# Kernel tuning notes

Hardware: AMD Instinct MI355X
Metric: run time of the kernel (lower is better)

The kernel has to match this reference:

```python
import jax, jax.numpy as jnp
import numpy as np

B, N, C, H, NL, NH = 8, 1024, 256, 512, 3, 8


def setup_inputs() -> dict:
    key = jax.random.key(0)
    ks = jax.random.split(key, 16)
    g = lambda k, shape: jax.random.normal(k, shape, jnp.float32) * 0.02
    return dict(
        concept_features=jax.random.normal(ks[0], (B, N, C), jnp.float32),
        adjacency_matrix=jax.random.uniform(ks[1], (B, N, N), jnp.float32),
        edge_types=jax.random.randint(ks[2], (B, N, N), 0, 10),
        concept_mask=jnp.ones((B, N), bool),
        W_emb=g(ks[3], (H, C)), b_emb=jnp.zeros((H,), jnp.float32),
        W_in=g(ks[4], (NL, 3 * H, H)), b_in=jnp.zeros((NL, 3 * H), jnp.float32),
        W_out=g(ks[5], (NL, H, H)), b_out=jnp.zeros((NL, H), jnp.float32),
        W_conv=g(ks[6], (NL, H, H)), b_conv=jnp.zeros((NL, H), jnp.float32),
        W_cls=g(ks[7], (1, H)), b_cls=jnp.zeros((1,), jnp.float32),
        W_diff=g(ks[8], (5, H)), b_diff=jnp.zeros((5,), jnp.float32),
        W_pre=g(ks[9], (1, 2 * H)), b_pre=jnp.zeros((1,), jnp.float32),
        W_pool=g(ks[10], (H, H)), b_pool=jnp.zeros((H,), jnp.float32),
    )


def reference(concept_features, adjacency_matrix, edge_types, concept_mask,
              W_emb, b_emb, W_in, b_in, W_out, b_out, W_conv, b_conv,
              W_cls, b_cls, W_diff, b_diff, W_pre, b_pre, W_pool, b_pool):
    Bq, Nc, _ = concept_features.shape
    Hd = W_emb.shape[0]
    dh = Hd // NH

    def mha(x, Wi, bi, Wo, bo):
        # torch nn.MultiheadAttention with batch_first=False: the (B,N,H)
        # input is treated as (seq=B, batch=N, embed=H) -> attention over B.
        qkv = x @ Wi.T + bi                      # (B,N,3H)
        q, k, v = jnp.split(qkv, 3, axis=-1)
        rs = lambda t: t.reshape(Bq, Nc, NH, dh)
        q, k, v = rs(q), rs(k), rs(v)
        sc = jnp.einsum('inhd,jnhd->nhij', q, k) / jnp.sqrt(jnp.float32(dh))
        a = jax.nn.softmax(sc, axis=-1)          # (N,NH,B,B)
        o = jnp.einsum('nhij,jnhd->inhd', a, v).reshape(Bq, Nc, Hd)
        return o @ Wo.T + bo

    def ln(x):  # F.layer_norm, no affine
        m = x.mean(-1, keepdims=True)
        v = ((x - m) ** 2).mean(-1, keepdims=True)
        return (x - m) * jax.lax.rsqrt(v + 1e-5)

    x = concept_features @ W_emb.T + b_emb       # (B,N,H)
    for l in range(W_in.shape[0]):
        att = mha(x, W_in[l], b_in[l], W_out[l], b_out[l])
        conv = att @ W_conv[l].T + b_conv[l]
        agg = jnp.einsum('bij,bjh->bih', adjacency_matrix, conv)
        x = ln(x + agg)

    mastery = x @ W_cls.T + b_cls                # (B,N,1)
    diff = x @ W_diff.T + b_diff                 # (B,N,5)

    # O(N^2) pairwise loop -> bilinear decomposition:
    # score(i,j) = x_i @ W_pre[:, :H].T + x_j @ W_pre[:, H:].T + b
    h1 = (x @ W_pre[:, :Hd].T)[..., 0]           # (B,N)
    h2 = (x @ W_pre[:, Hd:].T)[..., 0]           # (B,N)
    pair = h1[:, :, None] + h2[:, None, :] + b_pre[0]  # (B,N,N)
    off = ~np.eye(Nc, dtype=bool).reshape(-1)    # static mask, i!=j row-major
    prereq = pair.reshape(Bq, Nc * Nc)[:, off][..., None]  # (B,N*(N-1),1)

    graph = x.mean(axis=1) @ W_pool.T + b_pool   # (B,H)
    return (x, mastery, diff, prereq, graph)
```

## Files before the change

### kernel.cpp

```cpp
#include <hip/hip_runtime.h>
#include <hip/hip_bf16.h>

typedef unsigned short ushort_t;
typedef __attribute__((ext_vector_type(4))) float floatx4;
typedef __attribute__((ext_vector_type(8))) __bf16 bf16x8;
typedef __attribute__((ext_vector_type(4))) unsigned short ushortx4;
typedef __attribute__((ext_vector_type(8))) unsigned short ushortx8;

static __device__ __forceinline__ float b2f(ushort_t u) {
  union { unsigned int i; float f; } v; v.i = ((unsigned int)u) << 16; return v.f;
}
static __device__ __forceinline__ ushort_t f2b(float f) {
  unsigned int x = __float_as_uint(f);
  unsigned int r = (x + 0x7fffu + ((x >> 16) & 1u)) >> 16;
  return (ushort_t)r;
}
static __device__ __forceinline__ void glds16(const ushort_t* g, ushort_t* l) {
  __builtin_amdgcn_global_load_lds(
      (const __attribute__((address_space(1))) unsigned int*)g,
      (__attribute__((address_space(3))) unsigned int*)l, 16, 0, 0);
}

template<int MODE, bool ASPLIT, int KS>
__global__ __launch_bounds__(256, 3) void gemm_bt(
    const void* __restrict__ Ap, const ushort_t* __restrict__ Bm,
    const float* __restrict__ bias,
    ushort_t* __restrict__ C0, ushort_t* __restrict__ C1,
    ushort_t* __restrict__ C2, ushort_t* __restrict__ C3,
    int M, int N, int K, long aBatch, long bBatch, long cBatch)
{
  __shared__ __align__(16) ushort_t As[128 * 64];
  __shared__ __align__(16) ushort_t Bs[128 * 64];

  const int tid  = threadIdx.x;
  const int wid  = tid >> 6;
  const int lane = tid & 63;
  const int quad = lane >> 4;
  const int l16  = lane & 15;
  const int lin = blockIdx.y * gridDim.x + blockIdx.x;
  const int m0 = (lin % gridDim.y) * 128;
  const int n0 = (lin / gridDim.y) * 128;
  const int z  = (KS > 1) ? (int)(blockIdx.z / KS) : blockIdx.z;
  const int kq = (KS > 1) ? (int)(blockIdx.z % KS) : 0;
  const int kbeg = kq * (K / KS);
  const int kend = kbeg + (K / KS);
  ushort_t* outB = C0;
  if (KS >= 2 && kq == 1) outB = C1;
  if (KS >= 4 && kq == 2) outB = C2;
  if (KS >= 4 && kq == 3) outB = C3;

  const ushort_t* Ab = (const ushort_t*)Ap + (long)z * aBatch;
  const float*    Af = (const float*)Ap + (long)z * aBatch;
  Bm += (long)z * bBatch;

  const int wr = (wid >> 1) * 64;
  const int wc = (wid & 1) * 64;

  const int srow = tid >> 3;
  const int scj  = ((tid & 7) ^ (srow & 7)) * 8;
  const long abase = (long)(m0 + srow) * K + scj;
  const long bbase = (long)(n0 + srow) * K + scj;

  floatx4 acc[4][4];
#pragma unroll
  for (int i = 0; i < 4; ++i)
#pragma unroll
    for (int j = 0; j < 4; ++j) acc[i][j] = (floatx4){0.f, 0.f, 0.f, 0.f};

  const int rx = l16 & 7;

  for (int k0 = kbeg; k0 < kend; k0 += 64) {
    __syncthreads();
    if constexpr (ASPLIT) {
#pragma unroll
      for (int p = 0; p < 4; ++p)
        glds16(Ab + abase + 32 * p * (long)K + k0, &As[tid * 8 + p * 2048]);
    } else {
#pragma unroll
      for (int p = 0; p < 8; ++p) {
        int c = tid + p * 256;
        int row = c >> 4, sub4 = c & 15;
        floatx4 va = *(const floatx4*)(Af + (long)(m0 + row) * K + k0 + sub4 * 4);
        ushortx4 ah;
#pragma unroll
        for (int r = 0; r < 4; ++r) ah[r] = f2b(va[r]);
        int dst = row * 64 + (((sub4 >> 1) ^ (row & 7)) << 3) + ((sub4 & 1) << 2);
        *(ushortx4*)(&As[dst]) = ah;
      }
    }
#pragma unroll
    for (int p = 0; p < 4; ++p)
      glds16(Bm + bbase + 32 * p * (long)K + k0, &Bs[tid * 8 + p * 2048]);
    __syncthreads();

#pragma unroll
    for (int kk = 0; kk < 2; ++kk) {
      bf16x8 a[4], b[4];
#pragma unroll
      for (int i = 0; i < 4; ++i)
        a[i] = *(const bf16x8*)(&As[(wr + i * 16 + l16) * 64 +
                                    (((kk * 4 + quad) ^ rx) << 3)]);
#pragma unroll
      for (int j = 0; j < 4; ++j)
        b[j] = *(const bf16x8*)(&Bs[(wc + j * 16 + l16) * 64 +
                                    (((kk * 4 + quad) ^ rx) << 3)]);
#pragma unroll
      for (int i = 0; i < 4; ++i)
#pragma unroll
        for (int j = 0; j < 4; ++j)
          acc[i][j] = __builtin_amdgcn_mfma_f32_16x16x32_bf16(a[i], b[j], acc[i][j], 0, 0, 0);
    }
  }

#pragma unroll
  for (int j = 0; j < 4; ++j) {
    int col = n0 + wc + j * 16 + l16;
    float bv = (bias != nullptr) ? bias[col] : 0.f;
#pragma unroll
    for (int i = 0; i < 4; ++i) {
      int mbase = m0 + wr + i * 16 + quad * 4;
      if constexpr (MODE == 1) {
#pragma unroll
        for (int r = 0; r < 4; ++r)
          outB[(long)z * cBatch + (long)(mbase + r) * N + col] = f2b(acc[i][j][r] + bv);
      } else {
        int b = mbase >> 10, jrow = mbase & 1023;
        ushortx4 pk;
#pragma unroll
        for (int r = 0; r < 4; ++r) pk[r] = f2b(acc[i][j][r] + bv);
        *(ushortx4*)(outB + ((long)b * N + col) * 1024 + jrow) = pk;
      }
    }
  }
}

__global__ __launch_bounds__(256) void prep_kernel(
    const float* __restrict__ Win,  ushort_t* __restrict__ Winb,
    const float* __restrict__ Wemb, ushort_t* __restrict__ Wembb,
    const float* __restrict__ Wconv, ushort_t* __restrict__ Wcb,
    const float* __restrict__ ADJ,  ushort_t* __restrict__ ADJb,
    float* __restrict__ xm,
    const float* __restrict__ Wout, ushort_t* __restrict__ WoT,
    const float* __restrict__ bout, const float* __restrict__ bconv,
    float* __restrict__ bfused)
{
  __shared__ float tile[64][65];
  const int bid = blockIdx.x, tid = threadIdx.x;
  if (bid < 5696) {
    const float* src; ushort_t* dst; long i;
    if (bid < 1152)      { src = Win;   dst = Winb;  i = (long)bid * 256 + tid; }
    else if (bid < 1216) { src = Wemb;  dst = Wembb; i = (long)(bid - 1152) * 256 + tid; }
    else if (bid < 1600) { src = Wconv; dst = Wcb;   i = (long)(bid - 1216) * 256 + tid; }
    else                 { src = ADJ;   dst = ADJb;  i = (long)(bid - 1600) * 256 + tid; }
    floatx4 a = ((const floatx4*)src)[2 * i];
    floatx4 b = ((const floatx4*)src)[2 * i + 1];
    ushortx4 ha, hb;
#pragma unroll
    for (int r = 0; r < 4; ++r) { ha[r] = f2b(a[r]); hb[r] = f2b(b[r]); }
    ((ushortx4*)dst)[2 * i] = ha; ((ushortx4*)dst)[2 * i + 1] = hb;
  } else if (bid < 5712) {
    xm[(bid - 5696) * 256 + tid] = 0.f;
  } else if (bid < 5904) {
    const int t = bid - 5712;
    const int z = t >> 6, k0 = ((t >> 3) & 7) * 64, j0 = (t & 7) * 64;
    const long base = (long)z * 262144;
#pragma unroll
    for (int p = 0; p < 16; ++p) {
      int idx = tid + p * 256;
      int jj = idx >> 6, kk = idx & 63;
      tile[jj][kk] = Wout[base + (long)(j0 + jj) * 512 + k0 + kk];
    }
    __syncthreads();
#pragma unroll
    for (int p = 0; p < 16; ++p) {
      int idx = tid + p * 256;
      int kk = idx >> 6, jj = idx & 63;
      WoT[base + (long)(k0 + kk) * 512 + j0 + jj] = f2b(tile[jj][kk]);
    }
  } else {
    const int w = tid >> 6, lane = tid & 63;
    const int gi = (bid - 5904) * 4 + w;
    const int l = gi >> 9, o = gi & 511;
    float p = 0.f;
#pragma unroll
    for (int k = 0; k < 8; ++k)
      p += Wconv[(long)l * 262144 + (long)o * 512 + lane + 64 * k] *
           bout[l * 512 + lane + 64 * k];
#pragma unroll
    for (int msk = 1; msk <= 32; msk <<= 1) p += __shfl_xor(p, msk);
    if (lane == 0) bfused[gi] = p + bconv[l * 512 + o];
  }
}

__global__ __launch_bounds__(512) void attn_kernel(
    const ushort_t* __restrict__ qkv, ushort_t* __restrict__ outp)
{
  __shared__ float qs[8 * 1540];
  __shared__ float aw[8][64];
  const int tid = threadIdx.x;
  const int n = blockIdx.x;

  const ushort_t* src = qkv + (long)n * 1536;
#pragma unroll
  for (int p = 0; p < 3; ++p) {
    int c = tid + p * 512;
    int i = c / 192, off = (c % 192) * 8;
    ushortx8 u = *(const ushortx8*)(src + (long)i * 1024 * 1536 + off);
    float* d = &qs[i * 1540 + off];
#pragma unroll
    for (int r = 0; r < 8; ++r) d[r] = b2f(u[r]);
  }
  __syncthreads();

  const int h    = tid >> 6;
  const int lane = tid & 63;
  const int i = lane >> 3, j = lane & 7;
  float s = 0.f;
#pragma unroll 8
  for (int d = 0; d < 64; ++d)
    s += qs[i * 1540 + h * 64 + d] * qs[j * 1540 + 512 + h * 64 + d];
  s *= 0.125f;

  float m = s;
  m = fmaxf(m, __shfl_xor(m, 1));
  m = fmaxf(m, __shfl_xor(m, 2));
  m = fmaxf(m, __shfl_xor(m, 4));
  float e = __expf(s - m);
  float sum = e;
  sum += __shfl_xor(sum, 1);
  sum += __shfl_xor(sum, 2);
  sum += __shfl_xor(sum, 4);
  aw[h][lane] = e / sum;

  const long ob = (long)n * 512 + h * 64 + lane;
#pragma unroll
  for (int ii = 0; ii < 8; ++ii) {
    float acc = 0.f;
#pragma unroll
    for (int jj = 0; jj < 8; ++jj)
      acc += aw[h][ii * 8 + jj] * qs[jj * 1540 + 1024 + h * 64 + lane];
    outp[ob + (long)ii * 1024 * 512] = f2b(acc);
  }
}

__global__ __launch_bounds__(256) void ln_kernel(
    const ushort_t* __restrict__ xb,
    const ushort_t* __restrict__ aggA, const ushort_t* __restrict__ aggB,
    const ushort_t* __restrict__ aggC, const ushort_t* __restrict__ aggD,
    ushort_t* __restrict__ outB)
{
  const int w = threadIdx.x >> 6, lane = threadIdx.x & 63;
  const long base = ((long)blockIdx.x * 4 + w) * 512;
  float v[8];
  float s = 0.f;
#pragma unroll
  for (int k = 0; k < 8; ++k) {
    long idx = base + lane + 64 * k;
    v[k] = b2f(xb[idx]) + b2f(aggA[idx]) + b2f(aggB[idx]) +
           b2f(aggC[idx]) + b2f(aggD[idx]);
    s += v[k];
  }
#pragma unroll
  for (int msk = 1; msk <= 32; msk <<= 1) s += __shfl_xor(s, msk);
  float mean = s * (1.f / 512.f);
  float vv = 0.f;
#pragma unroll
  for (int k = 0; k < 8; ++k) { float d = v[k] - mean; vv += d * d; }
#pragma unroll
  for (int msk = 1; msk <= 32; msk <<= 1) vv += __shfl_xor(vv, msk);
  float inv = rsqrtf(vv * (1.f / 512.f) + 1e-5f);
#pragma unroll
  for (int k = 0; k < 8; ++k)
    outB[base + lane + 64 * k] = f2b((v[k] - mean) * inv);
}

__global__ __launch_bounds__(256) void final_ln_heads_kernel(
    const ushort_t* __restrict__ xb,
    const ushort_t* __restrict__ aggA, const ushort_t* __restrict__ aggB,
    const ushort_t* __restrict__ aggC, const ushort_t* __restrict__ aggD,
    float* __restrict__ out_x,
    const float* __restrict__ Wcls, const float* __restrict__ bcls,
    const float* __restrict__ Wdiff, const float* __restrict__ bdiff,
    const float* __restrict__ Wpre,
    float* __restrict__ mastery, float* __restrict__ diff,
    float* __restrict__ h1, float* __restrict__ h2)
{
  const int w = threadIdx.x >> 6, lane = threadIdx.x & 63;
  const long row = (long)blockIdx.x * 4 + w;
  const long base = row * 512;
  float v[8];
  float s = 0.f;
#pragma unroll
  for (int k = 0; k < 8; ++k) {
    long idx = base + lane + 64 * k;
    v[k] = b2f(xb[idx]) + b2f(aggA[idx]) + b2f(aggB[idx]) +
           b2f(aggC[idx]) + b2f(aggD[idx]);
    s += v[k];
  }
#pragma unroll
  for (int msk = 1; msk <= 32; msk <<= 1) s += __shfl_xor(s, msk);
  float mean = s * (1.f / 512.f);
  float vv = 0.f;
#pragma unroll
  for (int k = 0; k < 8; ++k) { float d = v[k] - mean; vv += d * d; }
#pragma unroll
  for (int msk = 1; msk <= 32; msk <<= 1) vv += __shfl_xor(vv, msk);
  float inv = rsqrtf(vv * (1.f / 512.f) + 1e-5f);
#pragma unroll
  for (int k = 0; k < 8; ++k) {
    v[k] = (v[k] - mean) * inv;
    out_x[base + lane + 64 * k] = v[k];
  }
#pragma unroll
  for (int o = 0; o < 8; ++o) {
    const float* wp = (o == 0) ? Wcls
                    : (o <= 5) ? (Wdiff + (o - 1) * 512)
                    : (o == 6) ? Wpre : (Wpre + 512);
    float p = 0.f;
#pragma unroll
    for (int k = 0; k < 8; ++k) p += v[k] * wp[lane + 64 * k];
#pragma unroll
    for (int msk = 1; msk <= 32; msk <<= 1) p += __shfl_xor(p, msk);
    if (lane == 0) {
      if (o == 0)      mastery[row] = p + bcls[0];
      else if (o <= 5) diff[row * 5 + (o - 1)] = p + bdiff[o - 1];
      else if (o == 6) h1[row] = p;
      else             h2[row] = p;
    }
  }
}

__global__ __launch_bounds__(256) void epi_kernel(
    const float* __restrict__ h1, const float* __restrict__ h2,
    const float* __restrict__ bpre, float* __restrict__ outp,
    const float* __restrict__ x, float* __restrict__ xm)
{
  const int bid = blockIdx.x;
  if (bid < 8192) {
    const int b = bid >> 10, i = bid & 1023;
    const float base = h1[b * 1024 + i] + bpre[0];
    const long ob = (long)b * (1024 * 1023) + (long)i * 1023;
#pragma unroll
    for (int r = 0; r < 4; ++r) {
      int j = r * 256 + threadIdx.x;
      if (j == i) continue;
      int pos = (j < i) ? j : j - 1;
      outp[ob + pos] = base + h2[b * 1024 + j];
    }
  } else {
    const int pb = bid - 8192;
    const int b = pb >> 5, cc = (pb >> 4) & 1, ns = pb & 15;
    const int c = cc * 256 + threadIdx.x;
    float s = 0.f;
    for (int n = ns * 64; n < ns * 64 + 64; ++n)
      s += x[((long)b * 1024 + n) * 512 + c];
    atomicAdd(&xm[b * 512 + c], s);
  }
}

__global__ __launch_bounds__(256) void graph_kernel(
    const float* __restrict__ xm, const float* __restrict__ Wpool,
    const float* __restrict__ bpool, float* __restrict__ g)
{
  const int gi = blockIdx.x * 256 + threadIdx.x;
  const int b = gi >> 9, o = gi & 511;
  float s = 0.f;
  for (int hh = 0; hh < 512; ++hh) s += xm[b * 512 + hh] * Wpool[o * 512 + hh];
  g[gi] = s * (1.f / 1024.f) + bpool[o];
}

extern "C" void kernel_launch(void* const* d_in, const int* in_sizes, int n_in,
                              void* d_out, int out_size, void* d_ws, size_t ws_size,
                              hipStream_t stream)
{
  const float* CF    = (const float*)d_in[0];
  const float* ADJ   = (const float*)d_in[1];
  const float* Wemb  = (const float*)d_in[4];
  const float* bemb  = (const float*)d_in[5];
  const float* Win   = (const float*)d_in[6];
  const float* bin   = (const float*)d_in[7];
  const float* Wout  = (const float*)d_in[8];
  const float* bout  = (const float*)d_in[9];
  const float* Wconv = (const float*)d_in[10];
  const float* bconv = (const float*)d_in[11];
  const float* Wcls  = (const float*)d_in[12];
  const float* bcls  = (const float*)d_in[13];
  const float* Wdiff = (const float*)d_in[14];
  const float* bdiff = (const float*)d_in[15];
  const float* Wpre  = (const float*)d_in[16];
  const float* bpre  = (const float*)d_in[17];
  const float* Wpool = (const float*)d_in[18];
  const float* bpool = (const float*)d_in[19];

  ushort_t* W = (ushort_t*)d_ws;
  ushort_t* xb   = W;
  ushort_t* qkvb = W + 4194304;
  ushort_t* cT    = qkvb;
  ushort_t* aggA  = qkvb + 4194304;
  ushort_t* aggB  = qkvb + 8388608;
  ushort_t* WoT   = qkvb + 4194304;
  ushort_t* Wembb = qkvb + 4980736;
  ushort_t* Wcb   = qkvb + 5111808;
  ushort_t* Winb = W + 16777216;
  ushort_t* Wfb  = W + 19136512;
  ushort_t* ADJb = W + 19922944;
  float* bfused = (float*)(W + 28311552);
  float* h1     = bfused + 1536;
  float* h2     = h1 + 8192;
  float* xm     = h2 + 8192;

  float* out_x       = (float*)d_out;
  float* out_mastery = out_x + 4194304;
  float* out_diff    = out_mastery + 8192;
  float* out_prereq  = out_diff + 40960;
  float* out_graph   = out_prereq + 8380416;
  ushort_t* aob = (ushort_t*)out_x;
  ushort_t* aggC = (ushort_t*)out_prereq;
  ushort_t* aggD = (ushort_t*)out_prereq + 4194304;

  dim3 blk(256);

  prep_kernel<<<dim3(6288), blk, 0, stream>>>(
      Win, Winb, Wemb, Wembb, Wconv, Wcb, ADJ, ADJb, xm,
      Wout, WoT, bout, bconv, bfused);
  gemm_bt<1, true, 1><<<dim3(4, 4, 3), blk, 0, stream>>>(
      Wcb, WoT, nullptr, Wfb, nullptr, nullptr, nullptr,
      512, 512, 512, 262144, 262144, 262144);

  gemm_bt<1, false, 1><<<dim3(4, 64, 1), blk, 0, stream>>>(
      CF, Wembb, bemb, xb, nullptr, nullptr, nullptr, 8192, 512, 256, 0, 0, 0);

  for (int l = 0; l < 3; ++l) {
    gemm_bt<1, true, 1><<<dim3(12, 64, 1), blk, 0, stream>>>(
        xb, Winb + (long)l * 786432, bin + l * 1536,
        qkvb, nullptr, nullptr, nullptr, 8192, 1536, 512, 0, 0, 0);
    attn_kernel<<<dim3(1024), dim3(512), 0, stream>>>(qkvb, aob);
    gemm_bt<2, true, 1><<<dim3(4, 64, 1), blk, 0, stream>>>(
        aob, Wfb + (long)l * 262144, bfused + l * 512,
        cT, nullptr, nullptr, nullptr, 8192, 512, 512, 0, 0, 0);
    gemm_bt<1, true, 4><<<dim3(4, 8, 32), blk, 0, stream>>>(
        ADJb, cT, nullptr, aggA, aggB, aggC, aggD,
        1024, 512, 1024, 1048576, 524288, 524288);
    if (l < 2)
      ln_kernel<<<dim3(2048), blk, 0, stream>>>(xb, aggA, aggB, aggC, aggD, xb);
    else
      final_ln_heads_kernel<<<dim3(2048), blk, 0, stream>>>(
          xb, aggA, aggB, aggC, aggD, out_x, Wcls, bcls, Wdiff, bdiff, Wpre,
          out_mastery, out_diff, h1, h2);
  }

  epi_kernel<<<dim3(8448), blk, 0, stream>>>(h1, h2, bpre, out_prereq,
                                             out_x, xm);
  graph_kernel<<<dim3(16), blk, 0, stream>>>(xm, Wpool, bpool, out_graph);
}
```

Baseline: 453.8 us.

## Fold embedding into first QKV projection, halve adjacency split-K, precompute mean partials

Precomputes W_in[0]·W_emb and a fused bias so the first layer's QKV GEMM reads concept features directly with K=256 instead of K=512. The adjacency aggregation GEMM drops from split-K 4 to split-K 2, so LayerNorm reads two partial buffers instead of four. The final LN kernel writes per-block row sums, which lets the graph-pooling mean reduction run without atomics and without rereading the full output. This trades extra prep work and longer per-block K loops in the aggregation GEMM for less memory traffic.

Result: no change. 459.1 us (+1.2%).

```diff
diff --git a/kernel.cpp b/kernel.cpp
--- a/kernel.cpp
+++ b/kernel.cpp
@@ -139,10 +139,12 @@
     const float* __restrict__ Wemb, ushort_t* __restrict__ Wembb,
     const float* __restrict__ Wconv, ushort_t* __restrict__ Wcb,
     const float* __restrict__ ADJ,  ushort_t* __restrict__ ADJb,
-    float* __restrict__ xm,
     const float* __restrict__ Wout, ushort_t* __restrict__ WoT,
     const float* __restrict__ bout, const float* __restrict__ bconv,
-    float* __restrict__ bfused)
+    float* __restrict__ bfused,
+    ushort_t* __restrict__ WembT,
+    const float* __restrict__ bemb, const float* __restrict__ bin0,
+    float* __restrict__ bfq)
 {
   __shared__ float tile[64][65];
   const int bid = blockIdx.x, tid = threadIdx.x;
@@ -158,10 +160,8 @@
 #pragma unroll
     for (int r = 0; r < 4; ++r) { ha[r] = f2b(a[r]); hb[r] = f2b(b[r]); }
     ((ushortx4*)dst)[2 * i] = ha; ((ushortx4*)dst)[2 * i + 1] = hb;
-  } else if (bid < 5712) {
-    xm[(bid - 5696) * 256 + tid] = 0.f;
-  } else if (bid < 5904) {
-    const int t = bid - 5712;
+  } else if (bid < 5888) {
+    const int t = bid - 5696;
     const int z = t >> 6, k0 = ((t >> 3) & 7) * 64, j0 = (t & 7) * 64;
     const long base = (long)z * 262144;
 #pragma unroll
@@ -177,9 +177,25 @@
       int kk = idx >> 6, jj = idx & 63;
       WoT[base + (long)(k0 + kk) * 512 + j0 + jj] = f2b(tile[jj][kk]);
     }
-  } else {
+  } else if (bid < 5920) {
+    const int t = bid - 5888;
+    const int j0 = (t >> 2) * 64, k0 = (t & 3) * 64;
+#pragma unroll
+    for (int p = 0; p < 16; ++p) {
+      int idx = tid + p * 256;
+      int jj = idx >> 6, kk = idx & 63;
+      tile[jj][kk] = Wemb[(long)(j0 + jj) * 256 + k0 + kk];
+    }
+    __syncthreads();
+#pragma unroll
+    for (int p = 0; p < 16; ++p) {
+      int idx = tid + p * 256;
+      int kk = idx >> 6, jj = idx & 63;
+      WembT[(long)(k0 + kk) * 512 + j0 + jj] = f2b(tile[jj][kk]);
+    }
+  } else if (bid < 6304) {
     const int w = tid >> 6, lane = tid & 63;
-    const int gi = (bid - 5904) * 4 + w;
+    const int gi = (bid - 5920) * 4 + w;
     const int l = gi >> 9, o = gi & 511;
     float p = 0.f;
 #pragma unroll
@@ -189,6 +205,16 @@
 #pragma unroll
     for (int msk = 1; msk <= 32; msk <<= 1) p += __shfl_xor(p, msk);
     if (lane == 0) bfused[gi] = p + bconv[l * 512 + o];
+  } else {
+    const int w = tid >> 6, lane = tid & 63;
+    const int o = (bid - 6304) * 4 + w;
+    float p = 0.f;
+#pragma unroll
+    for (int k = 0; k < 8; ++k)
+      p += Win[(long)o * 512 + lane + 64 * k] * bemb[lane + 64 * k];
+#pragma unroll
+    for (int msk = 1; msk <= 32; msk <<= 1) p += __shfl_xor(p, msk);
+    if (lane == 0) bfq[o] = p + bin0[o];
   }
 }
 
@@ -246,7 +272,6 @@
 __global__ __launch_bounds__(256) void ln_kernel(
     const ushort_t* __restrict__ xb,
     const ushort_t* __restrict__ aggA, const ushort_t* __restrict__ aggB,
-    const ushort_t* __restrict__ aggC, const ushort_t* __restrict__ aggD,
     ushort_t* __restrict__ outB)
 {
   const int w = threadIdx.x >> 6, lane = threadIdx.x & 63;
@@ -256,8 +281,7 @@
 #pragma unroll
   for (int k = 0; k < 8; ++k) {
     long idx = base + lane + 64 * k;
-    v[k] = b2f(xb[idx]) + b2f(aggA[idx]) + b2f(aggB[idx]) +
-           b2f(aggC[idx]) + b2f(aggD[idx]);
+    v[k] = b2f(xb[idx]) + b2f(aggA[idx]) + b2f(aggB[idx]);
     s += v[k];
   }
 #pragma unroll
@@ -277,14 +301,15 @@
 __global__ __launch_bounds__(256) void final_ln_heads_kernel(
     const ushort_t* __restrict__ xb,
     const ushort_t* __restrict__ aggA, const ushort_t* __restrict__ aggB,
-    const ushort_t* __restrict__ aggC, const ushort_t* __restrict__ aggD,
     float* __restrict__ out_x,
     const float* __restrict__ Wcls, const float* __restrict__ bcls,
     const float* __restrict__ Wdiff, const float* __restrict__ bdiff,
     const float* __restrict__ Wpre,
     float* __restrict__ mastery, float* __restrict__ diff,
-    float* __restrict__ h1, float* __restrict__ h2)
-{
+    float* __restrict__ h1, float* __restrict__ h2,
+    float* __restrict__ xp)
+{
+  __shared__ float sp4[4][512];
   const int w = threadIdx.x >> 6, lane = threadIdx.x & 63;
   const long row = (long)blockIdx.x * 4 + w;
   const long base = row * 512;
@@ -293,8 +318,7 @@
 #pragma unroll
   for (int k = 0; k < 8; ++k) {
     long idx = base + lane + 64 * k;
-    v[k] = b2f(xb[idx]) + b2f(aggA[idx]) + b2f(aggB[idx]) +
-           b2f(aggC[idx]) + b2f(aggD[idx]);
+    v[k] = b2f(xb[idx]) + b2f(aggA[idx]) + b2f(aggB[idx]);
     s += v[k];
   }
 #pragma unroll
@@ -310,7 +334,12 @@
   for (int k = 0; k < 8; ++k) {
     v[k] = (v[k] - mean) * inv;
     out_x[base + lane + 64 * k] = v[k];
-  }
+    sp4[w][lane + 64 * k] = v[k];
+  }
+  __syncthreads();
+  for (int t = threadIdx.x; t < 512; t += 256)
+    xp[(long)blockIdx.x * 512 + t] =
+        sp4[0][t] + sp4[1][t] + sp4[2][t] + sp4[3][t];
 #pragma unroll
   for (int o = 0; o < 8; ++o) {
     const float* wp = (o == 0) ? Wcls
@@ -333,7 +362,7 @@
 __global__ __launch_bounds__(256) void epi_kernel(
     const float* __restrict__ h1, const float* __restrict__ h2,
     const float* __restrict__ bpre, float* __restrict__ outp,
-    const float* __restrict__ x, float* __restrict__ xm)
+    const float* __restrict__ xp, float* __restrict__ xm)
 {
   const int bid = blockIdx.x;
   if (bid < 8192) {
@@ -348,13 +377,12 @@
       outp[ob + pos] = base + h2[b * 1024 + j];
     }
   } else {
-    const int pb = bid - 8192;
-    const int b = pb >> 5, cc = (pb >> 4) & 1, ns = pb & 15;
-    const int c = cc * 256 + threadIdx.x;
+    const int gi = (bid - 8192) * 256 + threadIdx.x;
+    const int b = gi >> 9, c = gi & 511;
+    const float* p = xp + (long)b * 256 * 512 + c;
     float s = 0.f;
-    for (int n = ns * 64; n < ns * 64 + 64; ++n)
-      s += x[((long)b * 1024 + n) * 512 + c];
-    atomicAdd(&xm[b * 512 + c], s);
+    for (int q = 0; q < 256; ++q) s += p[q * 512];
+    xm[b * 512 + c] = s;
   }
 }
 
@@ -401,13 +429,17 @@
   ushort_t* WoT   = qkvb + 4194304;
   ushort_t* Wembb = qkvb + 4980736;
   ushort_t* Wcb   = qkvb + 5111808;
+  ushort_t* WembT = qkvb + 5898240;
   ushort_t* Winb = W + 16777216;
   ushort_t* Wfb  = W + 19136512;
   ushort_t* ADJb = W + 19922944;
-  float* bfused = (float*)(W + 28311552);
-  float* h1     = bfused + 1536;
+  ushort_t* Wie  = W + 28311552;
+  float* bfused = (float*)(W + 28704768);
+  float* bfq    = bfused + 1536;
+  float* h1     = bfq + 1536;
   float* h2     = h1 + 8192;
   float* xm     = h2 + 8192;
+  float* xp     = xm + 4096;
 
   float* out_x       = (float*)d_out;
   float* out_mastery = out_x + 4194304;
@@ -415,14 +447,15 @@
   float* out_prereq  = out_diff + 40960;
   float* out_graph   = out_prereq + 8380416;
   ushort_t* aob = (ushort_t*)out_x;
-  ushort_t* aggC = (ushort_t*)out_prereq;
-  ushort_t* aggD = (ushort_t*)out_prereq + 4194304;
 
   dim3 blk(256);
 
-  prep_kernel<<<dim3(6288), blk, 0, stream>>>(
-      Win, Winb, Wemb, Wembb, Wconv, Wcb, ADJ, ADJb, xm,
-      Wout, WoT, bout, bconv, bfused);
+  prep_kernel<<<dim3(6688), blk, 0, stream>>>(
+      Win, Winb, Wemb, Wembb, Wconv, Wcb, ADJ, ADJb,
+      Wout, WoT, bout, bconv, bfused, WembT, bemb, bin, bfq);
+  gemm_bt<1, true, 1><<<dim3(2, 12, 1), blk, 0, stream>>>(
+      Winb, WembT, nullptr, Wie, nullptr, nullptr, nullptr,
+      1536, 256, 512, 0, 0, 0);
   gemm_bt<1, true, 1><<<dim3(4, 4, 3), blk, 0, stream>>>(
       Wcb, WoT, nullptr, Wfb, nullptr, nullptr, nullptr,
       512, 512, 512, 262144, 262144, 262144);
@@ -431,25 +464,31 @@
       CF, Wembb, bemb, xb, nullptr, nullptr, nullptr, 8192, 512, 256, 0, 0, 0);
 
   for (int l = 0; l < 3; ++l) {
-    gemm_bt<1, true, 1><<<dim3(12, 64, 1), blk, 0, stream>>>(
-        xb, Winb + (long)l * 786432, bin + l * 1536,
-        qkvb, nullptr, nullptr, nullptr, 8192, 1536, 512, 0, 0, 0);
+    if (l == 0) {
+      gemm_bt<1, false, 1><<<dim3(12, 64, 1), blk, 0, stream>>>(
+          CF, Wie, bfq, qkvb, nullptr, nullptr, nullptr,
+          8192, 1536, 256, 0, 0, 0);
+    } else {
+      gemm_bt<1, true, 1><<<dim3(12, 64, 1), blk, 0, stream>>>(
+          xb, Winb + (long)l * 786432, bin + l * 1536,
+          qkvb, nullptr, nullptr, nullptr, 8192, 1536, 512, 0, 0, 0);
+    }
     attn_kernel<<<dim3(1024), dim3(512), 0, stream>>>(qkvb, aob);
     gemm_bt<2, true, 1><<<dim3(4, 64, 1), blk, 0, stream>>>(
         aob, Wfb + (long)l * 262144, bfused + l * 512,
         cT, nullptr, nullptr, nullptr, 8192, 512, 512, 0, 0, 0);
-    gemm_bt<1, true, 4><<<dim3(4, 8, 32), blk, 0, stream>>>(
-        ADJb, cT, nullptr, aggA, aggB, aggC, aggD,
+    gemm_bt<1, true, 2><<<dim3(4, 8, 16), blk, 0, stream>>>(
+        ADJb, cT, nullptr, aggA, aggB, nullptr, nullptr,
         1024, 512, 1024, 1048576, 524288, 524288);
     if (l < 2)
-      ln_kernel<<<dim3(2048), blk, 0, stream>>>(xb, aggA, aggB, aggC, aggD, xb);
+      ln_kernel<<<dim3(2048), blk, 0, stream>>>(xb, aggA, aggB, xb);
     else
       final_ln_heads_kernel<<<dim3(2048), blk, 0, stream>>>(
-          xb, aggA, aggB, aggC, aggD, out_x, Wcls, bcls, Wdiff, bdiff, Wpre,
-          out_mastery, out_diff, h1, h2);
-  }
-
-  epi_kernel<<<dim3(8448), blk, 0, stream>>>(h1, h2, bpre, out_prereq,
-                                             out_x, xm);
+          xb, aggA, aggB, out_x, Wcls, bcls, Wdiff, bdiff, Wpre,
+          out_mastery, out_diff, h1, h2, xp);
+  }
+
+  epi_kernel<<<dim3(8208), blk, 0, stream>>>(h1, h2, bpre, out_prereq,
+                                             xp, xm);
   graph_kernel<<<dim3(16), blk, 0, stream>>>(xm, Wpool, bpool, out_graph);
 }
```
